# Kernel optimization log

Measured on AMD Instinct MI355X. Metric: run time of the kernel, lower is better.

Reference implementation:

```python
import jax, jax.numpy as jnp
import numpy as np

B, T, D = 2, 2048, 2048
H, KV = 16, 4
HD = D // H            # 128
REP = H // KV          # 4 query heads per kv head


def setup_inputs() -> dict:
    key = jax.random.key(0)
    ks = jax.random.split(key, 5)
    scale = D ** -0.5
    x = jax.random.normal(ks[0], (B, T, D), dtype=jnp.float32)
    Wq = jax.random.normal(ks[1], (D, H * HD), dtype=jnp.float32) * scale
    Wk = jax.random.normal(ks[2], (D, KV * HD), dtype=jnp.float32) * scale
    Wv = jax.random.normal(ks[3], (D, KV * HD), dtype=jnp.float32) * scale
    Wo = jax.random.normal(ks[4], (H * HD, D), dtype=jnp.float32) * scale
    return {"x": x, "Wq": Wq, "Wk": Wk, "Wv": Wv, "Wo": Wo}


def reference(x, Wq, Wk, Wv, Wo):
    b, t, d = x.shape
    # projections; group query heads by their kv head (repeat_interleave order:
    # q head h uses kv head h // REP, i.e. heads are contiguous per group)
    q = (x @ Wq).reshape(b, t, KV, REP, HD)          # bt(g r)d -> b t g r d
    k = (x @ Wk).reshape(b, t, KV, HD)
    v = (x @ Wv).reshape(b, t, KV, HD)
    # scores: [B, KV, REP, T, T] -- equivalent to repeat_interleave of kv heads
    scores = jnp.einsum('btgrd,bsgd->bgrts', q, k) * (HD ** -0.5)
    causal = jnp.tril(jnp.ones((t, t), dtype=bool))
    scores = jnp.where(causal, scores, -jnp.inf)
    weights = jax.nn.softmax(scores, axis=-1)
    out = jnp.einsum('bgrts,bsgd->btgrd', weights, v).reshape(b, t, H * HD)
    return jnp.round(out @ Wo, decimals=4)
```

## Files before the change

### kernel.cpp

```cpp
#include <hip/hip_runtime.h>
#include <hip/hip_bf16.h>
#include <math.h>

#define B_ 2
#define T_ 2048
#define D_ 2048
#define H_ 16
#define KV_ 4
#define HD_ 128
#define REP_ 4
#define QKVSTR 3072

typedef __attribute__((ext_vector_type(8))) short s16x8;
typedef __attribute__((ext_vector_type(4))) float f32x4;
typedef __hip_bfloat16 bf16;

__device__ __forceinline__ short f2bf(float x) {
    bf16 h = __float2bfloat16(x);
    return *reinterpret_cast<short*>(&h);
}

__device__ __forceinline__ void gl2lds16(const void* g, void* l) {
    __builtin_amdgcn_global_load_lds(
        (const __attribute__((address_space(1))) char*)g,
        (__attribute__((address_space(3))) char*)l, 16, 0, 0);
}

__global__ __launch_bounds__(256) void cast_bf16(const float* __restrict__ X,
                                                 bf16* __restrict__ Y, int n) {
    int i = (blockIdx.x * 256 + threadIdx.x) * 8;
    if (i >= n) return;
    float4 a = *(const float4*)(X + i);
    float4 b = *(const float4*)(X + i + 4);
    short o[8] = {f2bf(a.x), f2bf(a.y), f2bf(a.z), f2bf(a.w),
                  f2bf(b.x), f2bf(b.y), f2bf(b.z), f2bf(b.w)};
    *(s16x8*)(Y + i) = *(const s16x8*)o;
}

__global__ __launch_bounds__(256) void transpose_cast(const float* __restrict__ W,
                                                      bf16* __restrict__ Wt,
                                                      int K, int N, float scale) {
    __shared__ short tile[64 * 72];
    const int k0 = blockIdx.x * 64, n0 = blockIdx.y * 64;
    const int t = threadIdx.x;
    const int r = t >> 2, c0 = (t & 3) * 16;
    const float* src = W + (size_t)(k0 + r) * N + n0 + c0;
    #pragma unroll
    for (int i = 0; i < 16; i += 4) {
        float4 v = *(const float4*)(src + i);
        tile[r * 72 + c0 + i + 0] = f2bf(v.x * scale);
        tile[r * 72 + c0 + i + 1] = f2bf(v.y * scale);
        tile[r * 72 + c0 + i + 2] = f2bf(v.z * scale);
        tile[r * 72 + c0 + i + 3] = f2bf(v.w * scale);
    }
    __syncthreads();
    short tmp[16];
    #pragma unroll
    for (int i = 0; i < 16; ++i) tmp[i] = tile[(c0 + i) * 72 + r];
    bf16* dst = Wt + (size_t)(n0 + r) * K + k0 + c0;
    *(s16x8*)(dst)     = *(const s16x8*)&tmp[0];
    *(s16x8*)(dst + 8) = *(const s16x8*)&tmp[8];
}

__global__ __launch_bounds__(256) void transpose_v(const bf16* __restrict__ V,
                                                   bf16* __restrict__ Vtg) {
    __shared__ short tile[64 * 72];
    const int t0 = blockIdx.x * 64;
    const int g = blockIdx.y >> 1;
    const int dp = (blockIdx.y & 1) * 64;
    const int b = blockIdx.z;
    const int t = threadIdx.x;
    const int r = t >> 2, c0 = (t & 3) * 16;
    const bf16* src = V + (size_t)(b * T_ + t0 + r) * QKVSTR + g * HD_ + dp + c0;
    *(s16x8*)&tile[r * 72 + c0]     = *(const s16x8*)(src);
    *(s16x8*)&tile[r * 72 + c0 + 8] = *(const s16x8*)(src + 8);
    __syncthreads();
    const int d = t >> 2, tc = (t & 3) * 16;
    short tmp[16];
    #pragma unroll
    for (int i = 0; i < 16; ++i) tmp[i] = tile[(tc + i) * 72 + d];
    bf16* dst = Vtg + (size_t)((b * KV_ + g) * HD_ + dp + d) * T_ + t0 + tc;
    *(s16x8*)(dst)     = *(const s16x8*)&tmp[0];
    *(s16x8*)(dst + 8) = *(const s16x8*)&tmp[8];
}

template<typename OUTT, int ROUND>
__global__ __launch_bounds__(256) void gemm_nt(const bf16* __restrict__ A,
                                               const bf16* __restrict__ Bt,
                                               OUTT* __restrict__ C,
                                               int M, int N, int K) {
    __shared__ short As[128 * 64];
    __shared__ short Bs[128 * 64];
    const int tid = threadIdx.x;
    const int lane = tid & 63;
    const int wave = tid >> 6;
    const int quad = lane >> 4;
    const int l16 = lane & 15;
    const int wr = wave >> 1, wc = wave & 1;
    const int row0 = blockIdx.y * 128;
    const int col0 = blockIdx.x * 128;

    f32x4 acc[4][4] = {};

    for (int k0 = 0; k0 < K; k0 += 64) {
        __syncthreads();
        #pragma unroll
        for (int i = 0; i < 4; ++i) {
            int g = i * 256 + tid;
            int row = g >> 3;
            int cs = (g & 7) ^ (row & 7);
            gl2lds16(A + (size_t)(row0 + row) * K + k0 + cs * 8, &As[g * 8]);
        }
        #pragma unroll
        for (int i = 0; i < 4; ++i) {
            int g = i * 256 + tid;
            int row = g >> 3;
            int cs = (g & 7) ^ (row & 7);
            gl2lds16(Bt + (size_t)(col0 + row) * K + k0 + cs * 8, &Bs[g * 8]);
        }
        __syncthreads();
        #pragma unroll
        for (int kk = 0; kk < 2; ++kk) {
            s16x8 af[4], bfr[4];
            #pragma unroll
            for (int i = 0; i < 4; ++i) {
                int row = wr * 64 + i * 16 + l16;
                int c = (kk * 4 + quad) ^ (row & 7);
                af[i] = *(const s16x8*)&As[row * 64 + c * 8];
            }
            #pragma unroll
            for (int j = 0; j < 4; ++j) {
                int row = wc * 64 + j * 16 + l16;
                int c = (kk * 4 + quad) ^ (row & 7);
                bfr[j] = *(const s16x8*)&Bs[row * 64 + c * 8];
            }
            #pragma unroll
            for (int i = 0; i < 4; ++i)
                #pragma unroll
                for (int j = 0; j < 4; ++j)
                    acc[i][j] = __builtin_amdgcn_mfma_f32_16x16x32_bf16(
                        af[i], bfr[j], acc[i][j], 0, 0, 0);
        }
    }

    #pragma unroll
    for (int i = 0; i < 4; ++i) {
        #pragma unroll
        for (int j = 0; j < 4; ++j) {
            #pragma unroll
            for (int r = 0; r < 4; ++r) {
                int row = row0 + wr * 64 + i * 16 + quad * 4 + r;
                int col = col0 + wc * 64 + j * 16 + l16;
                float v = acc[i][j][r];
                if (ROUND) v = rintf(v * 1e4f) * 1e-4f;
                if constexpr (sizeof(OUTT) == 2)
                    C[(size_t)row * N + col] = __float2bfloat16(v);
                else
                    C[(size_t)row * N + col] = v;
            }
        }
    }
}

__global__ __launch_bounds__(256, 3) void flash3(const bf16* __restrict__ Q,
                                                 const bf16* __restrict__ K,
                                                 const bf16* __restrict__ Vtg,
                                                 bf16* __restrict__ O) {
    __shared__ short Kt[64 * 128];
    __shared__ short Vt[128 * 64];
    __shared__ short PsOb[64 * 136];
    __shared__ float lbuf[4][16];

    const int h = blockIdx.x;
    const int b = blockIdx.y & 1;
    const int qt = 31 - (blockIdx.y >> 1);
    const int g = h >> 2;
    const int tid = threadIdx.x;
    const int lane = tid & 63;
    const int wave = tid >> 6;
    const int quad = lane >> 4;
    const int l16 = lane & 15;
    const int q0g = qt * 64 + wave * 16;

    s16x8 qf[4];
    {
        const bf16* qp = Q + (size_t)(b * T_ + q0g + l16) * QKVSTR + h * HD_ + quad * 8;
        #pragma unroll
        for (int ks = 0; ks < 4; ++ks) qf[ks] = *(const s16x8*)(qp + ks * 32);
    }

    const bf16* Kp = K + (size_t)(b * T_) * QKVSTR + g * HD_;
    const bf16* Vp = Vtg + (size_t)((b * KV_ + g) * HD_) * T_;

    float l_part[4] = {0.f, 0.f, 0.f, 0.f};
    f32x4 oacc[8] = {};

    for (int j = 0; j <= qt; ++j) {
        const int s0 = j * 64;
        __syncthreads();
        #pragma unroll
        for (int i = 0; i < 4; ++i) {
            int g2 = i * 256 + tid;
            int s = g2 >> 4;
            int cs = (g2 & 15) ^ (s & 15);
            gl2lds16(Kp + (size_t)(s0 + s) * QKVSTR + cs * 8, &Kt[g2 * 8]);
        }
        #pragma unroll
        for (int i = 0; i < 4; ++i) {
            int g2 = i * 256 + tid;
            int d = g2 >> 3;
            int cs = (g2 & 7) ^ (d & 7);
            gl2lds16(Vp + (size_t)d * T_ + s0 + cs * 8, &Vt[g2 * 8]);
        }
        __syncthreads();

        f32x4 sacc[4] = {};
        #pragma unroll
        for (int ks = 0; ks < 4; ++ks) {
            s16x8 kf[4];
            #pragma unroll
            for (int ct = 0; ct < 4; ++ct) {
                int srow = ct * 16 + l16;
                int c = (ks * 4 + quad) ^ (srow & 15);
                kf[ct] = *(const s16x8*)&Kt[srow * 128 + c * 8];
            }
            #pragma unroll
            for (int ct = 0; ct < 4; ++ct)
                sacc[ct] = __builtin_amdgcn_mfma_f32_16x16x32_bf16(
                    qf[ks], kf[ct], sacc[ct], 0, 0, 0);
        }

        const bool diag = (j == qt);
        #pragma unroll
        for (int r = 0; r < 4; ++r) {
            const int qrow = q0g + quad * 4 + r;
            if (diag) {
                #pragma unroll
                for (int ct = 0; ct < 4; ++ct)
                    if (s0 + ct * 16 + l16 > qrow) sacc[ct][r] = -INFINITY;
            }
            float psum = 0.f;
            #pragma unroll
            for (int ct = 0; ct < 4; ++ct) {
                float p = exp2f(sacc[ct][r]);
                sacc[ct][r] = p;
                psum += p;
            }
            l_part[r] += psum;
        }

        #pragma unroll
        for (int ct = 0; ct < 4; ++ct)
            #pragma unroll
            for (int r = 0; r < 4; ++r)
                PsOb[(wave * 16 + quad * 4 + r) * 72 + ct * 16 + l16] = f2bf(sacc[ct][r]);

        #pragma unroll
        for (int kk = 0; kk < 2; ++kk) {
            const s16x8 pf = *(const s16x8*)&PsOb[(wave * 16 + l16) * 72 + kk * 32 + quad * 8];
            #pragma unroll
            for (int dt = 0; dt < 8; ++dt) {
                int d = dt * 16 + l16;
                int c = (kk * 4 + quad) ^ (d & 7);
                const s16x8 vf = *(const s16x8*)&Vt[d * 64 + c * 8];
                oacc[dt] = __builtin_amdgcn_mfma_f32_16x16x32_bf16(
                    vf, pf, oacc[dt], 0, 0, 0);
            }
        }
    }

    #pragma unroll
    for (int r = 0; r < 4; ++r) {
        float v = l_part[r];
        v += __shfl_xor(v, 1);
        v += __shfl_xor(v, 2);
        v += __shfl_xor(v, 4);
        v += __shfl_xor(v, 8);
        l_part[r] = v;
    }
    if (l16 == 0) {
        #pragma unroll
        for (int r = 0; r < 4; ++r) lbuf[wave][quad * 4 + r] = l_part[r];
    }
    const float invl = 1.f / lbuf[wave][l16];

    __syncthreads();

    #pragma unroll
    for (int dt = 0; dt < 8; ++dt) {
        short tmp[4];
        #pragma unroll
        for (int r = 0; r < 4; ++r) tmp[r] = f2bf(oacc[dt][r] * invl);
        *(long long*)&PsOb[(wave * 16 + l16) * 136 + dt * 16 + quad * 4] =
            *(const long long*)tmp;
    }
    const int r2 = wave * 16 + (lane >> 2);
    bf16* op = O + (size_t)(b * T_ + qt * 64 + r2) * (H_ * HD_) + h * HD_;
    #pragma unroll
    for (int c = 0; c < 4; ++c) {
        int chunk = c * 4 + (lane & 3);
        *(s16x8*)(op + chunk * 8) = *(const s16x8*)&PsOb[r2 * 136 + chunk * 8];
    }
}

extern "C" void kernel_launch(void* const* d_in, const int* in_sizes, int n_in,
                              void* d_out, int out_size, void* d_ws, size_t ws_size,
                              hipStream_t stream) {
    const float* x  = (const float*)d_in[0];
    const float* Wq = (const float*)d_in[1];
    const float* Wk = (const float*)d_in[2];
    const float* Wv = (const float*)d_in[3];
    const float* Wo = (const float*)d_in[4];
    float* out = (float*)d_out;

    const size_t NR = (size_t)B_ * T_;
    bf16* ws = (bf16*)d_ws;
    bf16* xb    = ws;
    bf16* Wqkvt = xb + NR * D_;
    bf16* Wot   = Wqkvt + (size_t)QKVSTR * D_;
    bf16* QKVb  = Wot + (size_t)D_ * D_;
    bf16* Vtg   = QKVb + NR * QKVSTR;
    bf16* Ab    = Vtg + (size_t)B_ * KV_ * HD_ * T_;

    const float qscale = 1.4426950408889634f / sqrtf((float)HD_);

    cast_bf16<<<4096, 256, 0, stream>>>(x, xb, (int)(NR * D_));
    transpose_cast<<<dim3(32, 32), 256, 0, stream>>>(Wq, Wqkvt, D_, H_ * HD_, qscale);
    transpose_cast<<<dim3(32, 8),  256, 0, stream>>>(Wk, Wqkvt + (size_t)2048 * D_, D_, KV_ * HD_, 1.f);
    transpose_cast<<<dim3(32, 8),  256, 0, stream>>>(Wv, Wqkvt + (size_t)2560 * D_, D_, KV_ * HD_, 1.f);
    transpose_cast<<<dim3(32, 32), 256, 0, stream>>>(Wo, Wot, H_ * HD_, D_, 1.f);

    gemm_nt<bf16, 0><<<dim3(QKVSTR / 128, NR / 128), 256, 0, stream>>>(
        xb, Wqkvt, QKVb, (int)NR, QKVSTR, D_);

    transpose_v<<<dim3(T_ / 64, 8, B_), 256, 0, stream>>>(QKVb + 2560, Vtg);

    flash3<<<dim3(H_, 64, 1), 256, 0, stream>>>(QKVb, QKVb + 2048, Vtg, Ab);

    gemm_nt<float, 1><<<dim3(D_ / 128, NR / 128), 256, 0, stream>>>(
        Ab, Wot, out, (int)NR, D_, H_ * HD_);
}
```

Before: 290.7 us.

## Merge prep kernels into one launch and fuse V transpose into QKV GEMM epilogue

The x cast and the four weight transpose-casts now run as one kernel that dispatches on block index, which removes four kernel launches. The separate V transpose kernel is gone: the QKV GEMM epilogue writes V columns directly in transposed per-group layout as packed 4-element stores. This removes a kernel launch and a re-read of V from global memory. The cost is extra scattered stores in the GEMM epilogue.

Measured after the change: 286.7 us. Within noise of the previous version (-1.4%).

```diff
diff --git a/kernel.cpp b/kernel.cpp
--- a/kernel.cpp
+++ b/kernel.cpp
@@ -12,6 +12,7 @@
 #define QKVSTR 3072
 
 typedef __attribute__((ext_vector_type(8))) short s16x8;
+typedef __attribute__((ext_vector_type(4))) short s16x4;
 typedef __attribute__((ext_vector_type(4))) float f32x4;
 typedef __hip_bfloat16 bf16;
 
@@ -26,23 +27,33 @@
         (__attribute__((address_space(3))) char*)l, 16, 0, 0);
 }
 
-__global__ __launch_bounds__(256) void cast_bf16(const float* __restrict__ X,
-                                                 bf16* __restrict__ Y, int n) {
-    int i = (blockIdx.x * 256 + threadIdx.x) * 8;
-    if (i >= n) return;
-    float4 a = *(const float4*)(X + i);
-    float4 b = *(const float4*)(X + i + 4);
-    short o[8] = {f2bf(a.x), f2bf(a.y), f2bf(a.z), f2bf(a.w),
-                  f2bf(b.x), f2bf(b.y), f2bf(b.z), f2bf(b.w)};
-    *(s16x8*)(Y + i) = *(const s16x8*)o;
-}
-
-__global__ __launch_bounds__(256) void transpose_cast(const float* __restrict__ W,
-                                                      bf16* __restrict__ Wt,
-                                                      int K, int N, float scale) {
+__global__ __launch_bounds__(256) void prep(const float* __restrict__ x,
+                                            const float* __restrict__ Wq,
+                                            const float* __restrict__ Wk,
+                                            const float* __restrict__ Wv,
+                                            const float* __restrict__ Wo,
+                                            bf16* __restrict__ xb,
+                                            bf16* __restrict__ Wqkvt,
+                                            bf16* __restrict__ Wot,
+                                            float qscale) {
+    const int bid = blockIdx.x;
+    const int t = threadIdx.x;
+    if (bid < 4096) {
+        int i = (bid * 256 + t) * 8;
+        float4 a = *(const float4*)(x + i);
+        float4 b = *(const float4*)(x + i + 4);
+        short o[8] = {f2bf(a.x), f2bf(a.y), f2bf(a.z), f2bf(a.w),
+                      f2bf(b.x), f2bf(b.y), f2bf(b.z), f2bf(b.w)};
+        *(s16x8*)(xb + i) = *(const s16x8*)o;
+        return;
+    }
     __shared__ short tile[64 * 72];
-    const int k0 = blockIdx.x * 64, n0 = blockIdx.y * 64;
-    const int t = threadIdx.x;
+    const float* W; bf16* dst; int N; float scale; int seg;
+    if (bid < 5120)      { seg = bid - 4096; W = Wq; dst = Wqkvt;                      N = 2048; scale = qscale; }
+    else if (bid < 5376) { seg = bid - 5120; W = Wk; dst = Wqkvt + (size_t)2048 * D_;  N = 512;  scale = 1.f; }
+    else if (bid < 5632) { seg = bid - 5376; W = Wv; dst = Wqkvt + (size_t)2560 * D_;  N = 512;  scale = 1.f; }
+    else                 { seg = bid - 5632; W = Wo; dst = Wot;                        N = 2048; scale = 1.f; }
+    const int k0 = (seg & 31) * 64, n0 = (seg >> 5) * 64;
     const int r = t >> 2, c0 = (t & 3) * 16;
     const float* src = W + (size_t)(k0 + r) * N + n0 + c0;
     #pragma unroll
@@ -57,37 +68,16 @@
     short tmp[16];
     #pragma unroll
     for (int i = 0; i < 16; ++i) tmp[i] = tile[(c0 + i) * 72 + r];
-    bf16* dst = Wt + (size_t)(n0 + r) * K + k0 + c0;
-    *(s16x8*)(dst)     = *(const s16x8*)&tmp[0];
-    *(s16x8*)(dst + 8) = *(const s16x8*)&tmp[8];
-}
-
-__global__ __launch_bounds__(256) void transpose_v(const bf16* __restrict__ V,
-                                                   bf16* __restrict__ Vtg) {
-    __shared__ short tile[64 * 72];
-    const int t0 = blockIdx.x * 64;
-    const int g = blockIdx.y >> 1;
-    const int dp = (blockIdx.y & 1) * 64;
-    const int b = blockIdx.z;
-    const int t = threadIdx.x;
-    const int r = t >> 2, c0 = (t & 3) * 16;
-    const bf16* src = V + (size_t)(b * T_ + t0 + r) * QKVSTR + g * HD_ + dp + c0;
-    *(s16x8*)&tile[r * 72 + c0]     = *(const s16x8*)(src);
-    *(s16x8*)&tile[r * 72 + c0 + 8] = *(const s16x8*)(src + 8);
-    __syncthreads();
-    const int d = t >> 2, tc = (t & 3) * 16;
-    short tmp[16];
-    #pragma unroll
-    for (int i = 0; i < 16; ++i) tmp[i] = tile[(tc + i) * 72 + d];
-    bf16* dst = Vtg + (size_t)((b * KV_ + g) * HD_ + dp + d) * T_ + t0 + tc;
-    *(s16x8*)(dst)     = *(const s16x8*)&tmp[0];
-    *(s16x8*)(dst + 8) = *(const s16x8*)&tmp[8];
-}
-
-template<typename OUTT, int ROUND>
+    bf16* d = dst + (size_t)(n0 + r) * D_ + k0 + c0;
+    *(s16x8*)(d)     = *(const s16x8*)&tmp[0];
+    *(s16x8*)(d + 8) = *(const s16x8*)&tmp[8];
+}
+
+template<typename OUTT, int ROUND, int WVT>
 __global__ __launch_bounds__(256) void gemm_nt(const bf16* __restrict__ A,
                                                const bf16* __restrict__ Bt,
                                                OUTT* __restrict__ C,
+                                               bf16* __restrict__ Vtg,
                                                int M, int N, int K) {
     __shared__ short As[128 * 64];
     __shared__ short Bs[128 * 64];
@@ -147,16 +137,28 @@
     for (int i = 0; i < 4; ++i) {
         #pragma unroll
         for (int j = 0; j < 4; ++j) {
+            const int col = col0 + wc * 64 + j * 16 + l16;
+            const int rowb = row0 + wr * 64 + i * 16 + quad * 4;
             #pragma unroll
             for (int r = 0; r < 4; ++r) {
-                int row = row0 + wr * 64 + i * 16 + quad * 4 + r;
-                int col = col0 + wc * 64 + j * 16 + l16;
                 float v = acc[i][j][r];
                 if (ROUND) v = rintf(v * 1e4f) * 1e-4f;
                 if constexpr (sizeof(OUTT) == 2)
-                    C[(size_t)row * N + col] = __float2bfloat16(v);
+                    C[(size_t)(rowb + r) * N + col] = __float2bfloat16(v);
                 else
-                    C[(size_t)row * N + col] = v;
+                    C[(size_t)(rowb + r) * N + col] = v;
+            }
+            if constexpr (WVT) {
+                if (col >= 2560) {
+                    const int dcol = (col - 2560) & 127;
+                    const int g = (col - 2560) >> 7;
+                    const int b = rowb >> 11;
+                    const int t = rowb & 2047;
+                    short pk[4] = {f2bf(acc[i][j][0]), f2bf(acc[i][j][1]),
+                                   f2bf(acc[i][j][2]), f2bf(acc[i][j][3])};
+                    *(s16x4*)&Vtg[(size_t)((b * KV_ + g) * HD_ + dcol) * T_ + t] =
+                        *(const s16x4*)pk;
+                }
             }
         }
     }
@@ -324,19 +326,13 @@
 
     const float qscale = 1.4426950408889634f / sqrtf((float)HD_);
 
-    cast_bf16<<<4096, 256, 0, stream>>>(x, xb, (int)(NR * D_));
-    transpose_cast<<<dim3(32, 32), 256, 0, stream>>>(Wq, Wqkvt, D_, H_ * HD_, qscale);
-    transpose_cast<<<dim3(32, 8),  256, 0, stream>>>(Wk, Wqkvt + (size_t)2048 * D_, D_, KV_ * HD_, 1.f);
-    transpose_cast<<<dim3(32, 8),  256, 0, stream>>>(Wv, Wqkvt + (size_t)2560 * D_, D_, KV_ * HD_, 1.f);
-    transpose_cast<<<dim3(32, 32), 256, 0, stream>>>(Wo, Wot, H_ * HD_, D_, 1.f);
-
-    gemm_nt<bf16, 0><<<dim3(QKVSTR / 128, NR / 128), 256, 0, stream>>>(
-        xb, Wqkvt, QKVb, (int)NR, QKVSTR, D_);
-
-    transpose_v<<<dim3(T_ / 64, 8, B_), 256, 0, stream>>>(QKVb + 2560, Vtg);
-
-    flash3<<<dim3(H_, 64, 1), 256, 0, stream>>>(QKVb, QKVb + 2048, Vtg, Ab);
-
-    gemm_nt<float, 1><<<dim3(D_ / 128, NR / 128), 256, 0, stream>>>(
-        Ab, Wot, out, (int)NR, D_, H_ * HD_);
-}
+    prep<<<6656, 256, 0, stream>>>(x, Wq, Wk, Wv, Wo, xb, Wqkvt, Wot, qscale);
+
+    gemm_nt<bf16, 0, 1><<<dim3(QKVSTR / 128, NR / 128), 256, 0, stream>>>(
+        xb, Wqkvt, QKVb, Vtg, (int)NR, QKVSTR, D_);
+
+    flash3<<<dim3(H_, 64), 256, 0, stream>>>(QKVb, QKVb + 2048, Vtg, Ab);
+
+    gemm_nt<float, 1, 0><<<dim3(D_ / 128, NR / 128), 256, 0, stream>>>(
+        Ab, Wot, out, nullptr, (int)NR, D_, H_ * HD_);
+}
```
